# Kernel tuning notes

Hardware: AMD Instinct MI355X
Metric: run time of the kernel (lower is better)

## Reference

```python
import jax, jax.numpy as jnp
import numpy as np
from jax import lax

RATIOS = (0.5, 1.0, 2.0)
SCALES = (8, 16, 32)
BASE = 16
STRIDE = 16
N_PRE = 6000
N_POST = 300      # post-NMS proposals kept
NMS_THRESH = 0.7
MIN_SIZE = 16.0


def _anchor_base():
    x = y = BASE / 2.0
    ab = np.zeros((len(RATIOS) * len(SCALES), 4), np.float32)
    for i, r in enumerate(RATIOS):
        for j, s in enumerate(SCALES):
            h = BASE * s * np.sqrt(r)
            w = BASE * s * np.sqrt(1.0 / r)
            k = i * len(SCALES) + j
            ab[k] = [y - h / 2, x - w / 2, y + h / 2, x + w / 2]
    return ab


def _anchors(h, w):
    ab = _anchor_base()
    sy = np.arange(0, h * STRIDE, STRIDE)
    sx = np.arange(0, w * STRIDE, STRIDE)
    sx, sy = np.meshgrid(sx, sy)
    shift = np.stack((sy.ravel(), sx.ravel(), sy.ravel(), sx.ravel()), axis=1)
    # [K, A, 4] -> [K*A, 4], row-major over (y, x) pixels matching NHWC flatten
    return (ab[None, :, :] + shift[:, None, :]).reshape(-1, 4).astype(np.float32)


def _conv(x, w, b, pad):
    y = lax.conv_general_dilated(x, w, (1, 1), ((pad, pad), (pad, pad)),
                                 dimension_numbers=('NCHW', 'OIHW', 'NCHW'))
    return y + b[None, :, None, None]


def _loc2bbox(anchor, loc):
    h = anchor[:, 2] - anchor[:, 0]
    w = anchor[:, 3] - anchor[:, 1]
    cy = anchor[:, 0] + 0.5 * h
    cx = anchor[:, 1] + 0.5 * w
    dy, dx, dh, dw = loc[:, 0], loc[:, 1], loc[:, 2], loc[:, 3]
    ncy = dy * h + cy
    ncx = dx * w + cx
    nh = jnp.exp(dh) * h
    nw = jnp.exp(dw) * w
    return jnp.stack([ncy - 0.5 * nh, ncx - 0.5 * nw, ncy + 0.5 * nh, ncx + 0.5 * nw], axis=1)


def _iou(b):
    tl = jnp.maximum(b[:, None, :2], b[None, :, :2])
    br = jnp.minimum(b[:, None, 2:], b[None, :, 2:])
    wh = jnp.clip(br - tl, 0.0)
    inter = wh[..., 0] * wh[..., 1]
    area = (b[:, 2] - b[:, 0]) * (b[:, 3] - b[:, 1])
    return inter / (area[:, None] + area[None, :] - inter + 1e-9)


def _nms_keep(iou):
    # greedy NMS over score-sorted boxes: suppress later boxes overlapping kept earlier ones
    n = iou.shape[0]
    idx = jnp.arange(n)
    def step(keep, i):
        sup = (iou[i] > NMS_THRESH) & (idx > i) & keep[i]
        return keep & (~sup), None
    keep, _ = lax.scan(step, jnp.ones((n,), dtype=bool), idx)
    return keep


def _proposal(loc, fg, anchor, img_h, img_w, scale=1.0):
    boxes = _loc2bbox(anchor, loc)
    boxes = jnp.stack([jnp.clip(boxes[:, 0], 0.0, img_h),
                       jnp.clip(boxes[:, 1], 0.0, img_w),
                       jnp.clip(boxes[:, 2], 0.0, img_h),
                       jnp.clip(boxes[:, 3], 0.0, img_w)], axis=1)
    hs = boxes[:, 2] - boxes[:, 0]
    ws = boxes[:, 3] - boxes[:, 1]
    ms = MIN_SIZE * scale
    score = jnp.where((hs >= ms) & (ws >= ms), fg, -jnp.inf)
    top, idx = lax.top_k(score, N_PRE)
    bk = boxes[idx]                                    # [N_PRE, 4]
    keep = _nms_keep(_iou(lax.stop_gradient(bk)))      # selection is non-differentiable
    fs = jnp.where(keep, top, -jnp.inf)
    _, o2 = lax.top_k(fs, N_POST)
    return bk[o2]                                      # [N_POST, 4]


def setup_inputs() -> dict:
    key = jax.random.key(0)
    ks = jax.random.split(key, 4)
    C, H, W = 512, 50, 76
    return {
        "feature": jax.random.normal(ks[0], (1, C, H, W), jnp.float32),
        "conv1_w": jax.random.normal(ks[1], (512, C, 3, 3), jnp.float32) * 0.01,
        "conv1_b": jnp.zeros((512,), jnp.float32),
        "score_w": jax.random.normal(ks[2], (18, 512, 1, 1), jnp.float32) * 0.01,
        "score_b": jnp.zeros((18,), jnp.float32),
        "loc_w": jax.random.normal(ks[3], (36, 512, 1, 1), jnp.float32) * 0.01,
        "loc_b": jnp.zeros((36,), jnp.float32),
        "img_h": 800,
        "img_w": 1216,
    }


def reference(feature, conv1_w, conv1_b, score_w, score_b, loc_w, loc_b, img_h, img_w):
    _, c, h, w = feature.shape
    A = 9
    anchor = jnp.asarray(_anchors(h, w))
    x = jax.nn.relu(_conv(feature, conv1_w, conv1_b, 1))
    locs = _conv(x, loc_w, loc_b, 0)
    rpn_locs = locs.transpose(0, 2, 3, 1).reshape(1, -1, 4)
    sc = _conv(x, score_w, score_b, 0).transpose(0, 2, 3, 1)   # [1, h, w, 2A]
    sm = jax.nn.softmax(sc.reshape(1, h, w, A, 2), axis=-1)
    fg = sm[..., 1].reshape(-1)
    rpn_scores = sc.reshape(1, -1, 2)
    rois = _proposal(rpn_locs[0], fg, anchor, float(img_h), float(img_w), scale=1.0)
    return rpn_locs, rpn_scores, rois, anchor
```

## Files before the change

### kernel.cpp

```cpp
#include <hip/hip_runtime.h>

#define HH 50
#define WW2 76
#define NPIX 3800
#define CIN 512
#define NANCH 34200
#define NPRE 6000
#define NPOST 300
#define WPR 94

typedef unsigned long long u64;
typedef unsigned int u32;

__global__ __launch_bounds__(256) void rpn_wtrans(const float* __restrict__ wgt,
                                                  float* __restrict__ wt,
                                                  u32* __restrict__ hist,
                                                  u32* __restrict__ info) {
    int id = blockIdx.x * 256 + threadIdx.x;
    if (id < 65536) hist[id] = 0u;
    else if (id < 65552) info[id - 65536] = 0u;
    int ko = id & 511;
    int tmp = id >> 9;
    int tap = tmp % 9, ci = tmp / 9;
    wt[id] = wgt[(size_t)ko * 4608 + ci * 9 + tap];
}

template <bool USEWT>
__global__ __launch_bounds__(256, 4) void rpn_conv1(
    const float* __restrict__ feat, const float* __restrict__ wsrc,
    float* __restrict__ Xp, int cin_blk) {
    const int yb = blockIdx.x;
    const int kg = blockIdx.y;
    const int cz = blockIdx.z;
    const int t  = threadIdx.x;
    const int kp = t & 31;
    const int ty = t >> 5;
    const int row  = ty >> 2;
    const int xseg = ty & 3;
    const int x0 = xseg * 20;
    __shared__ float in_l[2816];
    __shared__ float w_l[4608];

    const int y0 = yb * 2 - 1;
    int inSrc[11]; u32 inValid = 0, inPad = 0;
#pragma unroll
    for (int k = 0; k < 11; ++k) {
        int q = t + k * 256;
        int c = q / 336, rem = q - c * 336;
        int r = rem / 84, xx = rem - r * 84;
        int gy = y0 + r, gx = xx - 1;
        bool inb = q < 2688;
        bool ok = inb && ((unsigned)gy < 50u) && ((unsigned)gx < 76u);
        inSrc[k] = c * NPIX + gy * 76 + gx;
        if (ok) inValid |= (1u << k);
        else if (inb) inPad |= (1u << k);
    }
#pragma unroll
    for (int k = 0; k < 11; ++k)
        if ((inPad >> k) & 1) in_l[t + k * 256] = 0.f;

    const float* wb;
    int wOffA = 0;
    int wSrc[18];
    if (USEWT) {
        wb = wsrc + (size_t)(cz * cin_blk) * 9 * 512 + kg * 64;
        wOffA = 8 * t - 7 * (t & 63);
    } else {
        wb = wsrc + (size_t)(kg * 64) * 4608 + (size_t)(cz * cin_blk) * 9;
#pragma unroll
        for (int k = 0; k < 18; ++k) {
            int q = t + k * 256;
            int c = q / 576, r2 = q - c * 576;
            int tap = r2 >> 6, ko = r2 & 63;
            wSrc[k] = ko * 4608 + c * 9 + tap;
        }
    }

    const float* fb = feat + (size_t)(cz * cin_blk) * NPIX;
    float acc0[20], acc1[20];
#pragma unroll
    for (int p = 0; p < 20; ++p) { acc0[p] = 0.f; acc1[p] = 0.f; }

    const int niter = cin_blk >> 3;
#pragma unroll 1
    for (int it = 0; it < niter; ++it) {
        __syncthreads();
#pragma unroll
        for (int k = 0; k < 11; ++k)
            if ((inValid >> k) & 1) in_l[t + k * 256] = fb[inSrc[k]];
        if (USEWT) {
#pragma unroll
            for (int k = 0; k < 18; ++k)
                w_l[t + k * 256] = wb[wOffA + k * 2048];
        } else {
#pragma unroll
            for (int k = 0; k < 18; ++k)
                w_l[t + k * 256] = wb[wSrc[k]];
        }
        __syncthreads();
#pragma unroll 1
        for (int c = 0; c < 8; ++c) {
            const float* ir0 = &in_l[(c * 4 + row) * 84 + x0];
            const float* wl  = &w_l[c * 576 + 2 * kp];
#pragma unroll
            for (int r = 0; r < 3; ++r) {
                const float* ir = ir0 + r * 84;
                float win[22];
#pragma unroll
                for (int w = 0; w < 22; ++w) win[w] = ir[w];
                float w00 = wl[(r * 3 + 0) * 64],     w01 = wl[(r * 3 + 1) * 64],     w02 = wl[(r * 3 + 2) * 64];
                float w10 = wl[(r * 3 + 0) * 64 + 1], w11 = wl[(r * 3 + 1) * 64 + 1], w12 = wl[(r * 3 + 2) * 64 + 1];
#pragma unroll
                for (int p = 0; p < 20; ++p) {
                    acc0[p] = fmaf(w00, win[p],     acc0[p]);
                    acc0[p] = fmaf(w01, win[p + 1], acc0[p]);
                    acc0[p] = fmaf(w02, win[p + 2], acc0[p]);
                    acc1[p] = fmaf(w10, win[p],     acc1[p]);
                    acc1[p] = fmaf(w11, win[p + 1], acc1[p]);
                    acc1[p] = fmaf(w12, win[p + 2], acc1[p]);
                }
            }
        }
        fb += 8 * NPIX;
        wb += USEWT ? 8 * 9 * 512 : 72;
    }

    const int k0 = kg * 64 + 2 * kp;
    const int y = yb * 2 + row;
    float* d0 = Xp + ((size_t)cz * 512 + k0) * NPIX + y * 76 + x0;
#pragma unroll
    for (int p = 0; p < 20; p += 2) {
        if (x0 + p + 1 < 76) {
            *reinterpret_cast<float2*>(d0 + p)        = make_float2(acc0[p], acc0[p + 1]);
            *reinterpret_cast<float2*>(d0 + NPIX + p) = make_float2(acc1[p], acc1[p + 1]);
        }
    }
}

__global__ __launch_bounds__(256) void rpn_combine(
    const float* __restrict__ Xp, const float* __restrict__ bias,
    float* __restrict__ Xt, int nz) {
    const int p0 = blockIdx.x * 256;
    const int c0 = blockIdx.y * 16;
    const int t  = threadIdx.x;
    __shared__ float s[16][257];
    const int p = p0 + t;
#pragma unroll 4
    for (int i = 0; i < 16; ++i) {
        float v = 0.f;
        if (p < NPIX) {
            size_t base = (size_t)(c0 + i) * NPIX + p;
            float a = bias[c0 + i];
            for (int z = 0; z < nz; ++z) a += Xp[(size_t)z * 512 * NPIX + base];
            v = fmaxf(a, 0.f);
        }
        s[i][t] = v;
    }
    __syncthreads();
    const int cs = (t & 3) * 4;
    const int pr = t >> 2;
#pragma unroll
    for (int q = 0; q < 4; ++q) {
        int p2 = p0 + pr + q * 64;
        if (p2 < NPIX) {
            int pi = pr + q * 64;
            float4 v = make_float4(s[cs][pi], s[cs + 1][pi], s[cs + 2][pi], s[cs + 3][pi]);
            *reinterpret_cast<float4*>(&Xt[(size_t)p2 * 512 + c0 + cs]) = v;
        }
    }
}

__global__ __launch_bounds__(64) void rpn_head(
    const float* __restrict__ Xt,
    const float* __restrict__ sw, const float* __restrict__ sb,
    const float* __restrict__ lw, const float* __restrict__ lb,
    const int* __restrict__ ihp, const int* __restrict__ iwp,
    float* __restrict__ out, float* __restrict__ boxes,
    u32* __restrict__ keys, u32* __restrict__ hist) {
    const int p = blockIdx.x;
    const int t = threadIdx.x;
    __shared__ __align__(16) float xs[CIN];
    __shared__ float ov[64];
    const float4* xr = reinterpret_cast<const float4*>(Xt + (size_t)p * 512);
    reinterpret_cast<float4*>(xs)[t]      = xr[t];
    reinterpret_cast<float4*>(xs)[t + 64] = xr[t + 64];
    __syncthreads();
    if (t < 54) {
        const float* wr = (t < 18) ? (sw + t * CIN) : (lw + (t - 18) * CIN);
        float a = 0.f;
#pragma unroll 4
        for (int c = 0; c < CIN; c += 4) {
            float4 wv = *reinterpret_cast<const float4*>(wr + c);
            float4 xv = *reinterpret_cast<const float4*>(xs + c);
            a = fmaf(wv.x, xv.x, a); a = fmaf(wv.y, xv.y, a);
            a = fmaf(wv.z, xv.z, a); a = fmaf(wv.w, xv.w, a);
        }
        a += (t < 18) ? sb[t] : lb[t - 18];
        ov[t] = a;
    }
    __syncthreads();
    if (t < 9) {
        const int a = t;
        const float s0 = ov[2 * a], s1 = ov[2 * a + 1];
        const float dy = ov[18 + 4 * a], dx = ov[18 + 4 * a + 1];
        const float dh = ov[18 + 4 * a + 2], dw = ov[18 + 4 * a + 3];
        const int yy = p / WW2, xx = p % WW2;
        const int ai = p * 9 + a;
        *reinterpret_cast<float4*>(out + ai * 4) = make_float4(dy, dx, dh, dw);
        *reinterpret_cast<float2*>(out + 136800 + ai * 2) = make_float2(s0, s1);
        double r  = (a < 3) ? 0.5 : (a < 6) ? 1.0 : 2.0;
        int m3 = a % 3;
        double s2 = (m3 == 0) ? 8.0 : (m3 == 1) ? 16.0 : 32.0;
        double hd = (16.0 * s2) * sqrt(r);
        double wd = (16.0 * s2) * sqrt(1.0 / r);
        float ay1 = (float)(8.0 - hd * 0.5), ax1 = (float)(8.0 - wd * 0.5);
        float ay2 = (float)(8.0 + hd * 0.5), ax2 = (float)(8.0 + wd * 0.5);
        float fy = (float)(yy * 16), fx = (float)(xx * 16);
        float A0 = ay1 + fy, A1 = ax1 + fx, A2 = ay2 + fy, A3 = ax2 + fx;
        *reinterpret_cast<float4*>(out + 206400 + ai * 4) = make_float4(A0, A1, A2, A3);
        float ah = __fsub_rn(A2, A0), aw = __fsub_rn(A3, A1);
        float cy = __fadd_rn(A0, __fmul_rn(0.5f, ah));
        float cx = __fadd_rn(A1, __fmul_rn(0.5f, aw));
        float ncy = __fadd_rn(__fmul_rn(dy, ah), cy);
        float ncx = __fadd_rn(__fmul_rn(dx, aw), cx);
        float nh = __fmul_rn(expf(dh), ah);
        float nw = __fmul_rn(expf(dw), aw);
        float b0 = __fsub_rn(ncy, __fmul_rn(0.5f, nh));
        float b1 = __fsub_rn(ncx, __fmul_rn(0.5f, nw));
        float b2 = __fadd_rn(ncy, __fmul_rn(0.5f, nh));
        float b3 = __fadd_rn(ncx, __fmul_rn(0.5f, nw));
        const float ch = (float)(*ihp), cw = (float)(*iwp);
        b0 = fminf(fmaxf(b0, 0.f), ch); b2 = fminf(fmaxf(b2, 0.f), ch);
        b1 = fminf(fmaxf(b1, 0.f), cw); b3 = fminf(fmaxf(b3, 0.f), cw);
        float hs = __fsub_rn(b2, b0), wsz = __fsub_rn(b3, b1);
        float m = fmaxf(s0, s1);
        float e0 = expf(__fsub_rn(s0, m)), e1 = expf(__fsub_rn(s1, m));
        float fg = __fdiv_rn(e1, __fadd_rn(e0, e1));
        float score = (hs >= 16.f && wsz >= 16.f) ? fg : -__builtin_inff();
        *reinterpret_cast<float4*>(boxes + ai * 4) = make_float4(b0, b1, b2, b3);
        u32 kb = __float_as_uint(score);
        kb = (kb & 0x80000000u) ? ~kb : (kb | 0x80000000u);
        keys[ai] = kb;
        atomicAdd(&hist[kb >> 16], 1u);
    }
}

__global__ __launch_bounds__(256) void rpn_thresh(const u32* __restrict__ hist,
                                                  u32* __restrict__ info) {
    __shared__ u32 part[256], h2[256];
    __shared__ int segs;
    const int t = threadIdx.x;
    u32 s = 0;
    const u32* hp = hist + t * 256;
    for (int b = 0; b < 256; ++b) s += hp[b];
    part[t] = s;
    __syncthreads();
    for (int off = 1; off < 256; off <<= 1) {
        u32 v = part[t];
        u32 add = (t + off < 256) ? part[t + off] : 0u;
        __syncthreads();
        part[t] = v + add;
        __syncthreads();
    }
    u32 suf  = part[t];
    u32 sufn = (t < 255) ? part[t + 1] : 0u;
    if (suf >= NPRE && sufn < NPRE) segs = t;
    __syncthreads();
    const int seg = segs;
    const u32 above = (seg < 255) ? part[seg + 1] : 0u;
    h2[t] = hist[seg * 256 + t];
    __syncthreads();
    for (int off = 1; off < 256; off <<= 1) {
        u32 v = h2[t];
        u32 add = (t + off < 256) ? h2[t + off] : 0u;
        __syncthreads();
        h2[t] = v + add;
        __syncthreads();
    }
    u32 tot  = above + h2[t];
    u32 totn = above + ((t < 255) ? h2[t + 1] : 0u);
    if (tot >= NPRE && totn < NPRE) info[0] = (u32)(seg * 256 + t);
}

__global__ void rpn_select(const u32* __restrict__ keys, u32* __restrict__ info,
                           u64* __restrict__ selk) {
    int idx = blockIdx.x * 256 + threadIdx.x;
    if (idx >= NANCH) return;
    u32 k = keys[idx];
    if ((k >> 16) >= info[0]) {
        u32 pos = atomicAdd(&info[2], 1u);
        if (pos < 8192) selk[pos] = ((u64)k << 32) | (u64)(0xFFFFFFFFu - (u32)idx);
    }
}


__global__ __launch_bounds__(1024) void rpn_sort_local(u64* __restrict__ selk,
                                                       const u32* __restrict__ info) {
    __shared__ u64 s[2048];
    const int t = threadIdx.x;
    const int seg = blockIdx.x;
    const int base = seg * 2048;
    int n = (int)info[2]; if (n > 8192) n = 8192;
    for (int i = t; i < 2048; i += 1024) s[i] = (base + i < n) ? selk[base + i] : 0ull;
    __syncthreads();
    const bool D = ((seg & 1) == 0);
    for (int k = 2; k <= 2048; k <<= 1) {
        for (int j = k >> 1; j > 0; j >>= 1) {
            int p1 = ((t & ~(j - 1)) << 1) | (t & (j - 1));
            int p2 = p1 | j;
            bool desc = (((p1 & k) == 0) == D);
            u64 A = s[p1], B = s[p2];
            if (desc ? (A < B) : (A > B)) { s[p1] = B; s[p2] = A; }
            __syncthreads();
        }
    }
    for (int i = t; i < 2048; i += 1024) selk[base + i] = s[i];
}

__global__ __launch_bounds__(512) void rpn_sort_gpass(u64* __restrict__ selk,
                                                      int k, int j) {
    int i = blockIdx.x * 512 + threadIdx.x;
    int p1 = ((i & ~(j - 1)) << 1) | (i & (j - 1));
    int p2 = p1 | j;
    bool desc = ((p1 & k) == 0);
    u64 A = selk[p1], B = selk[p2];
    if (desc ? (A < B) : (A > B)) { selk[p1] = B; selk[p2] = A; }
}

template <bool FINAL>
__global__ __launch_bounds__(1024) void rpn_sort_lmerge(u64* __restrict__ selk, int k,
                                                        const float* __restrict__ boxes,
                                                        float* __restrict__ bk) {
    __shared__ u64 s[2048];
    const int t = threadIdx.x;
    const int seg = blockIdx.x;
    const int base = seg * 2048;
    for (int i = t; i < 2048; i += 1024) s[i] = selk[base + i];
    __syncthreads();
    const bool desc = ((base & k) == 0);
    for (int j = 1024; j > 0; j >>= 1) {
        int p1 = ((t & ~(j - 1)) << 1) | (t & (j - 1));
        int p2 = p1 | j;
        u64 A = s[p1], B = s[p2];
        if (desc ? (A < B) : (A > B)) { s[p1] = B; s[p2] = A; }
        __syncthreads();
    }
    if (FINAL) {
        for (int i = t; i < 2048; i += 1024) {
            int r = base + i;
            if (r < NPRE) {
                u32 oi = 0xFFFFFFFFu - (u32)(s[i] & 0xFFFFFFFFull);
                if (oi >= NANCH) oi = 0;
                reinterpret_cast<float4*>(bk)[r] = reinterpret_cast<const float4*>(boxes)[oi];
            }
        }
    } else {
        for (int i = t; i < 2048; i += 1024) selk[base + i] = s[i];
    }
}

__global__ __launch_bounds__(64) void rpn_iou(const float* __restrict__ bk,
                                              u64* __restrict__ mask) {
    const int t = threadIdx.x;
    const int bj = blockIdx.x, bi = blockIdx.y;
    const int j0 = bj * 64;
    const int i = bi * 64 + t;
    if (j0 + 63 <= bi * 64) {
        if (i < NPRE) mask[(size_t)i * WPR + bj] = 0ull;
        return;
    }
    __shared__ float4 jb[64];
    jb[t] = (j0 + t < NPRE) ? reinterpret_cast<const float4*>(bk)[j0 + t]
                            : make_float4(0.f, 0.f, 0.f, 0.f);
    __syncthreads();
    if (i >= NPRE) return;
    float4 b = reinterpret_cast<const float4*>(bk)[i];
    float areai = __fmul_rn(__fsub_rn(b.z, b.x), __fsub_rn(b.w, b.y));
    u64 bits = 0ull;
    for (int jj = 0; jj < 64; ++jj) {
        int j = j0 + jj;
        if (j <= i || j >= NPRE) continue;
        float4 c = jb[jj];
        float ty = fmaxf(b.x, c.x), tx = fmaxf(b.y, c.y);
        float by = fminf(b.z, c.z), bx2 = fminf(b.w, c.w);
        float ih = fmaxf(__fsub_rn(by, ty), 0.f);
        float iw = fmaxf(__fsub_rn(bx2, tx), 0.f);
        float inter = __fmul_rn(ih, iw);
        float areaj = __fmul_rn(__fsub_rn(c.z, c.x), __fsub_rn(c.w, c.y));
        float denom = __fadd_rn(__fsub_rn(__fadd_rn(areai, areaj), inter), 1e-9f);
        float iou = __fdiv_rn(inter, denom);
        if (iou > 0.7f) bits |= (1ull << jj);
    }
    mask[(size_t)i * WPR + bj] = bits;
}

__global__ __launch_bounds__(64) void rpn_nms(const u64* __restrict__ mask,
                                              const float* __restrict__ bk,
                                              float* __restrict__ rois) {
    const int lane = threadIdx.x;
    u64 rem0 = 0ull, rem1 = 0ull, curW = 0ull;
    __shared__ unsigned short klist[304];
    int kcnt = 0;
    u64 pm0[16], pm1[16], pmg[16];
#pragma unroll
    for (int u = 0; u < 16; ++u) {
        pm0[u] = mask[(size_t)u * WPR + lane];
        pm1[u] = (lane < 30) ? mask[(size_t)u * WPR + 64 + lane] : 0ull;
        pmg[u] = mask[(size_t)u * WPR + 0];
    }
    bool done = false;
    for (int base = 0; base < NPRE && !done; base += 16) {
        if ((base & 63) == 0) {
            int w = base >> 6;
            curW = (w < 64) ? __shfl(rem0, w) : __shfl(rem1, w - 64);
        }
#pragma unroll
        for (int u = 0; u < 16; ++u) {
            const int i = base + u;
            u64 m0 = pm0[u], m1 = pm1[u], mg = pmg[u];
            const int ni = i + 16;
            pm0[u] = mask[(size_t)ni * WPR + lane];
            pm1[u] = (lane < 30) ? mask[(size_t)ni * WPR + 64 + lane] : 0ull;
            pmg[u] = mask[(size_t)ni * WPR + (ni >> 6)];
            if (((curW >> (i & 63)) & 1ull) == 0ull) {
                rem0 |= m0;
                rem1 |= m1;
                curW |= mg;
                if (lane == 0 && kcnt < 304) klist[kcnt] = (unsigned short)i;
                ++kcnt;
                if (kcnt >= NPOST) { done = true; break; }
            }
        }
    }
    __syncthreads();
    const int nk = kcnt < NPOST ? kcnt : NPOST;
    for (int r = lane; r < nk; r += 64) {
        int bi = klist[r];
        reinterpret_cast<float4*>(rois)[r] = reinterpret_cast<const float4*>(bk)[bi];
    }
    if (kcnt < NPOST) {
        int pos = kcnt;
        for (int i = 0; i < NPRE && pos < NPOST; ++i) {
            int w = i >> 6;
            u64 wv = (w < 64) ? __shfl(rem0, w) : __shfl(rem1, w - 64);
            if ((wv >> (i & 63)) & 1ull) {
                if (lane < 4) rois[pos * 4 + lane] = bk[i * 4 + lane];
                ++pos;
            }
        }
    }
}

extern "C" void kernel_launch(void* const* d_in, const int* in_sizes, int n_in,
                              void* d_out, int out_size, void* d_ws, size_t ws_size,
                              hipStream_t stream) {
    (void)in_sizes; (void)n_in; (void)out_size;
    const float* feat = (const float*)d_in[0];
    const float* w1   = (const float*)d_in[1];
    const float* b1   = (const float*)d_in[2];
    const float* sw   = (const float*)d_in[3];
    const float* sb   = (const float*)d_in[4];
    const float* lw   = (const float*)d_in[5];
    const float* lb   = (const float*)d_in[6];
    const int*   ih   = (const int*)d_in[7];
    const int*   iw   = (const int*)d_in[8];
    float* out = (float*)d_out;

    const size_t WT_B    = 9437184;
    const size_t XT_B    = 7782400;
    const size_t REST_B  = 547200 + 136800 + 262144 + 64 + 65536 + 96000 + 4528128;
    const size_t SLICE_B = (size_t)512 * NPIX * 4;
    int nz; bool usewt;
    if      (ws_size >= 8 * SLICE_B + WT_B + XT_B + REST_B) { nz = 8; usewt = true; }
    else if (ws_size >= 4 * SLICE_B + WT_B + XT_B + REST_B) { nz = 4; usewt = true; }
    else if (ws_size >= 2 * SLICE_B + WT_B + XT_B + REST_B) { nz = 2; usewt = true; }
    else                                                    { nz = 2; usewt = false; }

    char* p = (char*)d_ws;
    float* Xp = (float*)p;           p += (size_t)nz * SLICE_B;
    float* wt = nullptr;
    if (usewt) { wt = (float*)p;     p += WT_B; }
    float* Xt     = (float*)p;       p += XT_B;
    float* boxes  = (float*)p;       p += 547200;
    u32*   keys   = (u32*)p;         p += 136800;
    u32*   hist   = (u32*)p;         p += 262144;
    u32*   info   = (u32*)p;         p += 64;
    u64*   selk   = (u64*)p;         p += 65536;
    float* bk     = (float*)p;       p += 96000;
    u64*   mask   = (u64*)p;

    const int cin_blk = 512 / nz;

    if (usewt) {
        rpn_wtrans<<<9216, 256, 0, stream>>>(w1, wt, hist, info);
        rpn_conv1<true><<<dim3(25, 8, nz), 256, 0, stream>>>(feat, wt, Xp, cin_blk);
    } else {
        rpn_wtrans<<<9216, 256, 0, stream>>>(w1, (float*)Xt, hist, info);
        rpn_conv1<false><<<dim3(25, 8, nz), 256, 0, stream>>>(feat, w1, Xp, cin_blk);
    }
    rpn_combine<<<dim3(15, 32), 256, 0, stream>>>(Xp, b1, Xt, nz);
    rpn_head<<<NPIX, 64, 0, stream>>>(Xt, sw, sb, lw, lb, ih, iw, out, boxes, keys, hist);
    rpn_thresh<<<1, 256, 0, stream>>>(hist, info);
    rpn_select<<<(NANCH + 255) / 256, 256, 0, stream>>>(keys, info, selk);
    rpn_sort_local<<<4, 1024, 0, stream>>>(selk, info);
    rpn_sort_gpass<<<8, 512, 0, stream>>>(selk, 4096, 2048);
    rpn_sort_lmerge<false><<<4, 1024, 0, stream>>>(selk, 4096, nullptr, nullptr);
    rpn_sort_gpass<<<8, 512, 0, stream>>>(selk, 8192, 4096);
    rpn_sort_gpass<<<8, 512, 0, stream>>>(selk, 8192, 2048);
    rpn_sort_lmerge<true><<<4, 1024, 0, stream>>>(selk, 8192, boxes, bk);
    rpn_iou<<<dim3(WPR, WPR), 64, 0, stream>>>(bk, mask);
    rpn_nms<<<1, 64, 0, stream>>>(mask, bk, out + 205200);
}
```

Measured before the change: 659.6 us.

## Prefetch conv tiles in registers, batch head pixels, tile weight transpose, pad sort LDS

```diff
diff --git a/kernel.cpp b/kernel.cpp
--- a/kernel.cpp
+++ b/kernel.cpp
@@ -12,17 +12,43 @@
 typedef unsigned long long u64;
 typedef unsigned int u32;
 
+__device__ __forceinline__ int PADL(int i) { return i + (i >> 4); }
+
+template <bool DOW>
 __global__ __launch_bounds__(256) void rpn_wtrans(const float* __restrict__ wgt,
                                                   float* __restrict__ wt,
+                                                  const float* __restrict__ sw,
+                                                  const float* __restrict__ lw,
+                                                  float* __restrict__ wt2,
                                                   u32* __restrict__ hist,
                                                   u32* __restrict__ info) {
-    int id = blockIdx.x * 256 + threadIdx.x;
-    if (id < 65536) hist[id] = 0u;
-    else if (id < 65552) info[id - 65536] = 0u;
-    int ko = id & 511;
-    int tmp = id >> 9;
-    int tap = tmp % 9, ci = tmp / 9;
-    wt[id] = wgt[(size_t)ko * 4608 + ci * 9 + tap];
+    __shared__ float tile[32][33];
+    const int bx = blockIdx.x;
+    const int by = blockIdx.y;
+    const int t  = threadIdx.x;
+    const int tx = t & 31, ty = t >> 5;
+    int gid = (by * 144 + bx) * 256 + t;
+    if (gid < 65536) hist[gid] = 0u;
+    else if (gid < 65552) info[gid - 65536] = 0u;
+    if (gid < 32768) {
+        int c = gid >> 6, n = gid & 63;
+        float v = 0.f;
+        if (n < 18) v = sw[n * 512 + c];
+        else if (n < 54) v = lw[(n - 18) * 512 + c];
+        wt2[((c >> 2) * 64 + n) * 4 + (c & 3)] = v;
+    }
+    if (!DOW) return;
+#pragma unroll
+    for (int r = 0; r < 32; r += 8) {
+        int ko = by * 32 + ty + r;
+        tile[ty + r][tx] = wgt[(size_t)ko * 4608 + bx * 32 + tx];
+    }
+    __syncthreads();
+#pragma unroll
+    for (int r = 0; r < 32; r += 8) {
+        int cit = bx * 32 + ty + r;
+        wt[(size_t)cit * 512 + by * 32 + tx] = tile[tx][ty + r];
+    }
 }
 
 template <bool USEWT>
@@ -81,23 +107,41 @@
 #pragma unroll
     for (int p = 0; p < 20; ++p) { acc0[p] = 0.f; acc1[p] = 0.f; }
 
+    float rin[11], rw[18];
+#pragma unroll
+    for (int k = 0; k < 11; ++k)
+        if ((inValid >> k) & 1) rin[k] = fb[inSrc[k]];
+    if (USEWT) {
+#pragma unroll
+        for (int k = 0; k < 18; ++k) rw[k] = wb[wOffA + k * 2048];
+    } else {
+#pragma unroll
+        for (int k = 0; k < 18; ++k) rw[k] = wb[wSrc[k]];
+    }
+
     const int niter = cin_blk >> 3;
 #pragma unroll 1
     for (int it = 0; it < niter; ++it) {
-        __syncthreads();
 #pragma unroll
         for (int k = 0; k < 11; ++k)
-            if ((inValid >> k) & 1) in_l[t + k * 256] = fb[inSrc[k]];
-        if (USEWT) {
-#pragma unroll
-            for (int k = 0; k < 18; ++k)
-                w_l[t + k * 256] = wb[wOffA + k * 2048];
-        } else {
-#pragma unroll
-            for (int k = 0; k < 18; ++k)
-                w_l[t + k * 256] = wb[wSrc[k]];
-        }
-        __syncthreads();
+            if ((inValid >> k) & 1) in_l[t + k * 256] = rin[k];
+#pragma unroll
+        for (int k = 0; k < 18; ++k) w_l[t + k * 256] = rw[k];
+        __syncthreads();
+        if (it + 1 < niter) {
+            fb += 8 * NPIX;
+            wb += USEWT ? 8 * 9 * 512 : 72;
+#pragma unroll
+            for (int k = 0; k < 11; ++k)
+                if ((inValid >> k) & 1) rin[k] = fb[inSrc[k]];
+            if (USEWT) {
+#pragma unroll
+                for (int k = 0; k < 18; ++k) rw[k] = wb[wOffA + k * 2048];
+            } else {
+#pragma unroll
+                for (int k = 0; k < 18; ++k) rw[k] = wb[wSrc[k]];
+            }
+        }
 #pragma unroll 1
         for (int c = 0; c < 8; ++c) {
             const float* ir0 = &in_l[(c * 4 + row) * 84 + x0];
@@ -121,8 +165,7 @@
                 }
             }
         }
-        fb += 8 * NPIX;
-        wb += USEWT ? 8 * 9 * 512 : 72;
+        __syncthreads();
     }
 
     const int k0 = kg * 64 + 2 * kp;
@@ -171,77 +214,93 @@
 }
 
 __global__ __launch_bounds__(64) void rpn_head(
-    const float* __restrict__ Xt,
-    const float* __restrict__ sw, const float* __restrict__ sb,
-    const float* __restrict__ lw, const float* __restrict__ lb,
+    const float* __restrict__ Xt, const float* __restrict__ wt2,
+    const float* __restrict__ sb, const float* __restrict__ lb,
     const int* __restrict__ ihp, const int* __restrict__ iwp,
     float* __restrict__ out, float* __restrict__ boxes,
     u32* __restrict__ keys, u32* __restrict__ hist) {
-    const int p = blockIdx.x;
-    const int t = threadIdx.x;
-    __shared__ __align__(16) float xs[CIN];
-    __shared__ float ov[64];
-    const float4* xr = reinterpret_cast<const float4*>(Xt + (size_t)p * 512);
-    reinterpret_cast<float4*>(xs)[t]      = xr[t];
-    reinterpret_cast<float4*>(xs)[t + 64] = xr[t + 64];
-    __syncthreads();
-    if (t < 54) {
-        const float* wr = (t < 18) ? (sw + t * CIN) : (lw + (t - 18) * CIN);
-        float a = 0.f;
+    const int p0 = blockIdx.x * 8;
+    const int t  = threadIdx.x;
+    __shared__ __align__(16) float xs[8 * 512];
+    __shared__ float ovl[8][64];
+    const float4* src = reinterpret_cast<const float4*>(Xt + (size_t)p0 * 512);
+    float4* dst = reinterpret_cast<float4*>(xs);
+#pragma unroll
+    for (int i = 0; i < 16; ++i) dst[t + i * 64] = src[t + i * 64];
+    __syncthreads();
+    float acc[8];
+    {
+        float b = (t < 18) ? sb[t] : ((t < 54) ? lb[t - 18] : 0.f);
+#pragma unroll
+        for (int px = 0; px < 8; ++px) acc[px] = b;
+    }
+    const float4* wv = reinterpret_cast<const float4*>(wt2) + t;
 #pragma unroll 4
-        for (int c = 0; c < CIN; c += 4) {
-            float4 wv = *reinterpret_cast<const float4*>(wr + c);
-            float4 xv = *reinterpret_cast<const float4*>(xs + c);
-            a = fmaf(wv.x, xv.x, a); a = fmaf(wv.y, xv.y, a);
-            a = fmaf(wv.z, xv.z, a); a = fmaf(wv.w, xv.w, a);
-        }
-        a += (t < 18) ? sb[t] : lb[t - 18];
-        ov[t] = a;
-    }
-    __syncthreads();
-    if (t < 9) {
-        const int a = t;
-        const float s0 = ov[2 * a], s1 = ov[2 * a + 1];
-        const float dy = ov[18 + 4 * a], dx = ov[18 + 4 * a + 1];
-        const float dh = ov[18 + 4 * a + 2], dw = ov[18 + 4 * a + 3];
-        const int yy = p / WW2, xx = p % WW2;
-        const int ai = p * 9 + a;
-        *reinterpret_cast<float4*>(out + ai * 4) = make_float4(dy, dx, dh, dw);
-        *reinterpret_cast<float2*>(out + 136800 + ai * 2) = make_float2(s0, s1);
-        double r  = (a < 3) ? 0.5 : (a < 6) ? 1.0 : 2.0;
-        int m3 = a % 3;
-        double s2 = (m3 == 0) ? 8.0 : (m3 == 1) ? 16.0 : 32.0;
-        double hd = (16.0 * s2) * sqrt(r);
-        double wd = (16.0 * s2) * sqrt(1.0 / r);
-        float ay1 = (float)(8.0 - hd * 0.5), ax1 = (float)(8.0 - wd * 0.5);
-        float ay2 = (float)(8.0 + hd * 0.5), ax2 = (float)(8.0 + wd * 0.5);
-        float fy = (float)(yy * 16), fx = (float)(xx * 16);
-        float A0 = ay1 + fy, A1 = ax1 + fx, A2 = ay2 + fy, A3 = ax2 + fx;
-        *reinterpret_cast<float4*>(out + 206400 + ai * 4) = make_float4(A0, A1, A2, A3);
-        float ah = __fsub_rn(A2, A0), aw = __fsub_rn(A3, A1);
-        float cy = __fadd_rn(A0, __fmul_rn(0.5f, ah));
-        float cx = __fadd_rn(A1, __fmul_rn(0.5f, aw));
-        float ncy = __fadd_rn(__fmul_rn(dy, ah), cy);
-        float ncx = __fadd_rn(__fmul_rn(dx, aw), cx);
-        float nh = __fmul_rn(expf(dh), ah);
-        float nw = __fmul_rn(expf(dw), aw);
-        float b0 = __fsub_rn(ncy, __fmul_rn(0.5f, nh));
-        float b1 = __fsub_rn(ncx, __fmul_rn(0.5f, nw));
-        float b2 = __fadd_rn(ncy, __fmul_rn(0.5f, nh));
-        float b3 = __fadd_rn(ncx, __fmul_rn(0.5f, nw));
-        const float ch = (float)(*ihp), cw = (float)(*iwp);
-        b0 = fminf(fmaxf(b0, 0.f), ch); b2 = fminf(fmaxf(b2, 0.f), ch);
-        b1 = fminf(fmaxf(b1, 0.f), cw); b3 = fminf(fmaxf(b3, 0.f), cw);
-        float hs = __fsub_rn(b2, b0), wsz = __fsub_rn(b3, b1);
-        float m = fmaxf(s0, s1);
-        float e0 = expf(__fsub_rn(s0, m)), e1 = expf(__fsub_rn(s1, m));
-        float fg = __fdiv_rn(e1, __fadd_rn(e0, e1));
-        float score = (hs >= 16.f && wsz >= 16.f) ? fg : -__builtin_inff();
-        *reinterpret_cast<float4*>(boxes + ai * 4) = make_float4(b0, b1, b2, b3);
-        u32 kb = __float_as_uint(score);
-        kb = (kb & 0x80000000u) ? ~kb : (kb | 0x80000000u);
-        keys[ai] = kb;
-        atomicAdd(&hist[kb >> 16], 1u);
+    for (int c4 = 0; c4 < 128; ++c4) {
+        float4 w = wv[c4 * 64];
+#pragma unroll
+        for (int px = 0; px < 8; ++px) {
+            float4 x = *reinterpret_cast<const float4*>(xs + px * 512 + c4 * 4);
+            acc[px] = fmaf(w.x, x.x, acc[px]);
+            acc[px] = fmaf(w.y, x.y, acc[px]);
+            acc[px] = fmaf(w.z, x.z, acc[px]);
+            acc[px] = fmaf(w.w, x.w, acc[px]);
+        }
+    }
+#pragma unroll
+    for (int px = 0; px < 8; ++px) ovl[px][t] = acc[px];
+    __syncthreads();
+    const float ch = (float)(*ihp), cw = (float)(*iwp);
+#pragma unroll
+    for (int pass = 0; pass < 2; ++pass) {
+        int a, px;
+        bool act;
+        if (pass == 0) { act = (t < 63); px = t / 9; a = t - px * 9; }
+        else           { act = (t < 9);  px = 7;     a = t; }
+        if (act) {
+            const int p = p0 + px;
+            const float* ov = ovl[px];
+            const float s0 = ov[2 * a], s1 = ov[2 * a + 1];
+            const float dy = ov[18 + 4 * a], dx = ov[18 + 4 * a + 1];
+            const float dh = ov[18 + 4 * a + 2], dw = ov[18 + 4 * a + 3];
+            const int yy = p / WW2, xx = p % WW2;
+            const int ai = p * 9 + a;
+            *reinterpret_cast<float4*>(out + ai * 4) = make_float4(dy, dx, dh, dw);
+            *reinterpret_cast<float2*>(out + 136800 + ai * 2) = make_float2(s0, s1);
+            double r  = (a < 3) ? 0.5 : (a < 6) ? 1.0 : 2.0;
+            int m3 = a % 3;
+            double s2 = (m3 == 0) ? 8.0 : (m3 == 1) ? 16.0 : 32.0;
+            double hd = (16.0 * s2) * sqrt(r);
+            double wd = (16.0 * s2) * sqrt(1.0 / r);
+            float ay1 = (float)(8.0 - hd * 0.5), ax1 = (float)(8.0 - wd * 0.5);
+            float ay2 = (float)(8.0 + hd * 0.5), ax2 = (float)(8.0 + wd * 0.5);
+            float fy = (float)(yy * 16), fx = (float)(xx * 16);
+            float A0 = ay1 + fy, A1 = ax1 + fx, A2 = ay2 + fy, A3 = ax2 + fx;
+            *reinterpret_cast<float4*>(out + 206400 + ai * 4) = make_float4(A0, A1, A2, A3);
+            float ah = __fsub_rn(A2, A0), aw = __fsub_rn(A3, A1);
+            float cy = __fadd_rn(A0, __fmul_rn(0.5f, ah));
+            float cx = __fadd_rn(A1, __fmul_rn(0.5f, aw));
+            float ncy = __fadd_rn(__fmul_rn(dy, ah), cy);
+            float ncx = __fadd_rn(__fmul_rn(dx, aw), cx);
+            float nh = __fmul_rn(expf(dh), ah);
+            float nw = __fmul_rn(expf(dw), aw);
+            float b0 = __fsub_rn(ncy, __fmul_rn(0.5f, nh));
+            float b1 = __fsub_rn(ncx, __fmul_rn(0.5f, nw));
+            float b2 = __fadd_rn(ncy, __fmul_rn(0.5f, nh));
+            float b3 = __fadd_rn(ncx, __fmul_rn(0.5f, nw));
+            b0 = fminf(fmaxf(b0, 0.f), ch); b2 = fminf(fmaxf(b2, 0.f), ch);
+            b1 = fminf(fmaxf(b1, 0.f), cw); b3 = fminf(fmaxf(b3, 0.f), cw);
+            float hs = __fsub_rn(b2, b0), wsz = __fsub_rn(b3, b1);
+            float m = fmaxf(s0, s1);
+            float e0 = expf(__fsub_rn(s0, m)), e1 = expf(__fsub_rn(s1, m));
+            float fg = __fdiv_rn(e1, __fadd_rn(e0, e1));
+            float score = (hs >= 16.f && wsz >= 16.f) ? fg : -__builtin_inff();
+            *reinterpret_cast<float4*>(boxes + ai * 4) = make_float4(b0, b1, b2, b3);
+            u32 kb = __float_as_uint(score);
+            kb = (kb & 0x80000000u) ? ~kb : (kb | 0x80000000u);
+            keys[ai] = kb;
+            atomicAdd(&hist[kb >> 16], 1u);
+        }
     }
 }
 
@@ -284,24 +343,29 @@
 
 __global__ void rpn_select(const u32* __restrict__ keys, u32* __restrict__ info,
                            u64* __restrict__ selk) {
-    int idx = blockIdx.x * 256 + threadIdx.x;
-    if (idx >= NANCH) return;
-    u32 k = keys[idx];
-    if ((k >> 16) >= info[0]) {
-        u32 pos = atomicAdd(&info[2], 1u);
+    const int idx = blockIdx.x * 256 + threadIdx.x;
+    const int lane = threadIdx.x & 63;
+    u32 k = (idx < NANCH) ? keys[idx] : 0u;
+    bool sel = (idx < NANCH) && ((k >> 16) >= info[0]);
+    u64 ball = __ballot(sel);
+    u32 base = 0;
+    if (lane == 0 && ball) base = atomicAdd(&info[2], (u32)__popcll(ball));
+    base = __shfl(base, 0);
+    if (sel) {
+        u32 pos = base + (u32)__popcll(ball & ((1ull << lane) - 1ull));
         if (pos < 8192) selk[pos] = ((u64)k << 32) | (u64)(0xFFFFFFFFu - (u32)idx);
     }
 }
-
 
 __global__ __launch_bounds__(1024) void rpn_sort_local(u64* __restrict__ selk,
                                                        const u32* __restrict__ info) {
-    __shared__ u64 s[2048];
+    __shared__ u64 s[2176];
     const int t = threadIdx.x;
     const int seg = blockIdx.x;
     const int base = seg * 2048;
     int n = (int)info[2]; if (n > 8192) n = 8192;
-    for (int i = t; i < 2048; i += 1024) s[i] = (base + i < n) ? selk[base + i] : 0ull;
+    for (int i = t; i < 2048; i += 1024)
+        s[PADL(i)] = (base + i < n) ? selk[base + i] : 0ull;
     __syncthreads();
     const bool D = ((seg & 1) == 0);
     for (int k = 2; k <= 2048; k <<= 1) {
@@ -309,12 +373,12 @@
             int p1 = ((t & ~(j - 1)) << 1) | (t & (j - 1));
             int p2 = p1 | j;
             bool desc = (((p1 & k) == 0) == D);
-            u64 A = s[p1], B = s[p2];
-            if (desc ? (A < B) : (A > B)) { s[p1] = B; s[p2] = A; }
+            u64 A = s[PADL(p1)], B = s[PADL(p2)];
+            if (desc ? (A < B) : (A > B)) { s[PADL(p1)] = B; s[PADL(p2)] = A; }
             __syncthreads();
         }
     }
-    for (int i = t; i < 2048; i += 1024) selk[base + i] = s[i];
+    for (int i = t; i < 2048; i += 1024) selk[base + i] = s[PADL(i)];
 }
 
 __global__ __launch_bounds__(512) void rpn_sort_gpass(u64* __restrict__ selk,
@@ -331,31 +395,30 @@
 __global__ __launch_bounds__(1024) void rpn_sort_lmerge(u64* __restrict__ selk, int k,
                                                         const float* __restrict__ boxes,
                                                         float* __restrict__ bk) {
-    __shared__ u64 s[2048];
+    __shared__ u64 s[2176];
     const int t = threadIdx.x;
-    const int seg = blockIdx.x;
-    const int base = seg * 2048;
-    for (int i = t; i < 2048; i += 1024) s[i] = selk[base + i];
+    const int base = blockIdx.x * 2048;
+    for (int i = t; i < 2048; i += 1024) s[PADL(i)] = selk[base + i];
     __syncthreads();
     const bool desc = ((base & k) == 0);
     for (int j = 1024; j > 0; j >>= 1) {
         int p1 = ((t & ~(j - 1)) << 1) | (t & (j - 1));
         int p2 = p1 | j;
-        u64 A = s[p1], B = s[p2];
-        if (desc ? (A < B) : (A > B)) { s[p1] = B; s[p2] = A; }
+        u64 A = s[PADL(p1)], B = s[PADL(p2)];
+        if (desc ? (A < B) : (A > B)) { s[PADL(p1)] = B; s[PADL(p2)] = A; }
         __syncthreads();
     }
     if (FINAL) {
         for (int i = t; i < 2048; i += 1024) {
             int r = base + i;
             if (r < NPRE) {
-                u32 oi = 0xFFFFFFFFu - (u32)(s[i] & 0xFFFFFFFFull);
+                u32 oi = 0xFFFFFFFFu - (u32)(s[PADL(i)] & 0xFFFFFFFFull);
                 if (oi >= NANCH) oi = 0;
                 reinterpret_cast<float4*>(bk)[r] = reinterpret_cast<const float4*>(boxes)[oi];
             }
         }
     } else {
-        for (int i = t; i < 2048; i += 1024) selk[base + i] = s[i];
+        for (int i = t; i < 2048; i += 1024) selk[base + i] = s[PADL(i)];
     }
 }
 
@@ -467,8 +530,9 @@
     float* out = (float*)d_out;
 
     const size_t WT_B    = 9437184;
+    const size_t WT2_B   = 131072;
     const size_t XT_B    = 7782400;
-    const size_t REST_B  = 547200 + 136800 + 262144 + 64 + 65536 + 96000 + 4528128;
+    const size_t REST_B  = WT2_B + 547200 + 136800 + 262144 + 64 + 65536 + 96000 + 4528128;
     const size_t SLICE_B = (size_t)512 * NPIX * 4;
     int nz; bool usewt;
     if      (ws_size >= 8 * SLICE_B + WT_B + XT_B + REST_B) { nz = 8; usewt = true; }
@@ -481,6 +545,7 @@
     float* wt = nullptr;
     if (usewt) { wt = (float*)p;     p += WT_B; }
     float* Xt     = (float*)p;       p += XT_B;
+    float* wt2    = (float*)p;       p += WT2_B;
     float* boxes  = (float*)p;       p += 547200;
     u32*   keys   = (u32*)p;         p += 136800;
     u32*   hist   = (u32*)p;         p += 262144;
@@ -492,14 +557,14 @@
     const int cin_blk = 512 / nz;
 
     if (usewt) {
-        rpn_wtrans<<<9216, 256, 0, stream>>>(w1, wt, hist, info);
+        rpn_wtrans<true><<<dim3(144, 16), 256, 0, stream>>>(w1, wt, sw, lw, wt2, hist, info);
         rpn_conv1<true><<<dim3(25, 8, nz), 256, 0, stream>>>(feat, wt, Xp, cin_blk);
     } else {
-        rpn_wtrans<<<9216, 256, 0, stream>>>(w1, (float*)Xt, hist, info);
+        rpn_wtrans<false><<<dim3(144, 16), 256, 0, stream>>>(w1, nullptr, sw, lw, wt2, hist, info);
         rpn_conv1<false><<<dim3(25, 8, nz), 256, 0, stream>>>(feat, w1, Xp, cin_blk);
     }
     rpn_combine<<<dim3(15, 32), 256, 0, stream>>>(Xp, b1, Xt, nz);
-    rpn_head<<<NPIX, 64, 0, stream>>>(Xt, sw, sb, lw, lb, ih, iw, out, boxes, keys, hist);
+    rpn_head<<<475, 64, 0, stream>>>(Xt, wt2, sb, lb, ih, iw, out, boxes, keys, hist);
     rpn_thresh<<<1, 256, 0, stream>>>(hist, info);
     rpn_select<<<(NANCH + 255) / 256, 256, 0, stream>>>(keys, info, selk);
     rpn_sort_local<<<4, 1024, 0, stream>>>(selk, info);
```

Measured after the change: 669.1 us. About the same (+1.4%).
